# Performance work log

Hardware: AMD Instinct MI355X
Metric: run time of the kernel (lower is better)

Reference implementation:

```python
import jax, jax.numpy as jnp
import numpy as np

B, V, S, H = 16384, 16, 64, 512


def setup_inputs() -> dict:
    key = jax.random.key(0)
    kx, kw, kb, kws, kbs = jax.random.split(key, 5)
    x = jax.random.normal(kx, (B, V, S), dtype=jnp.float32)
    # per-variable linear layers: weight [V, S, H], bias [V, H]
    W = jax.random.normal(kw, (V, S, H), dtype=jnp.float32) * (1.0 / np.sqrt(S))
    b = jax.random.normal(kb, (V, H), dtype=jnp.float32) * 0.01
    # variable selection linear: hidden -> V
    W_sel = jax.random.normal(kws, (H, V), dtype=jnp.float32) * (1.0 / np.sqrt(H))
    b_sel = jax.random.normal(kbs, (V,), dtype=jnp.float32) * 0.01
    return {"x": x, "W": W, "b": b, "W_sel": W_sel, "b_sel": b_sel}


def reference(x, W, b, W_sel, b_sel):
    # per-variable linears: [B, V, H]
    transformed = jnp.einsum('bvs,vsh->bvh', x, W) + b  # grouped small GEMMs
    # torch stacks to [B, H, V]; mean over variable axis -> [B, H]
    flat = transformed.mean(axis=1)
    # softmax-gated selection weights [B, V] (dropout is identity in eval)
    weights = jax.nn.softmax(flat @ W_sel + b_sel, axis=-1)
    # weighted sum over variables -> [B, H]
    out = jnp.einsum('bvh,bv->bh', transformed, weights)
    return out
```

## Files before the change

kernel.cpp:

```cpp
#include <hip/hip_runtime.h>
#include <hip/hip_bf16.h>
#include <stdint.h>

#define B_ROWS 16384
#define VDIM   16
#define SDIM   64
#define HDIM   512
#define KDIM   1024
#define KP     1056
#define ASTR   1064
#define K2_LDS (64 * ASTR * 2)

using bf16x8 = __attribute__((ext_vector_type(8))) __bf16;
using u16x8  = __attribute__((ext_vector_type(8))) unsigned short;
using f32x4  = __attribute__((ext_vector_type(4))) float;

__device__ __forceinline__ unsigned short f2bf(float f) {
  unsigned int u = __builtin_bit_cast(unsigned int, f);
  u = (u + 0x7FFFu + ((u >> 16) & 1u)) >> 16;
  return (unsigned short)u;
}
__device__ __forceinline__ float bf2f(unsigned short s) {
  return __builtin_bit_cast(float, (unsigned int)s << 16);
}

__global__ __launch_bounds__(256) void k0_prep(
    const float* __restrict__ W, const float* __restrict__ bias,
    const float* __restrict__ Wsel, const float* __restrict__ bsel,
    unsigned short* __restrict__ Bt, unsigned short* __restrict__ WcombT,
    float* __restrict__ bcomb) {
  __shared__ float bm[HDIM];
  __shared__ float part[16][17];
  const int t = threadIdx.x;
  if (blockIdx.x < 2112) {
    int idx = blockIdx.x * 256 + t;
    int k = idx >> 9;
    int n = idx & 511;
    float val;
    if (k < KDIM)            val = W[(size_t)k * HDIM + n];
    else if (k < KDIM + 16)  val = bias[(size_t)(k - KDIM) * HDIM + n];
    else                     val = 0.f;
    Bt[(size_t)n * KP + k] = f2bf(val);
    return;
  }
  const int bid = blockIdx.x - 2112;
  if (bid < 256) {
    const int wave = t >> 6, lane = t & 63;
    const int k = bid * 4 + wave;
    const float* wr = W + (size_t)k * HDIM;
    float s[16];
    #pragma unroll
    for (int v = 0; v < 16; ++v) s[v] = 0.f;
    #pragma unroll
    for (int j = 0; j < 8; ++j) {
      const int h = lane + 64 * j;
      const float a = wr[h];
      const float4* wl = (const float4*)(Wsel + h * 16);
      const float4 q0 = wl[0], q1 = wl[1], q2 = wl[2], q3 = wl[3];
      s[0]  = fmaf(a, q0.x, s[0]);  s[1]  = fmaf(a, q0.y, s[1]);
      s[2]  = fmaf(a, q0.z, s[2]);  s[3]  = fmaf(a, q0.w, s[3]);
      s[4]  = fmaf(a, q1.x, s[4]);  s[5]  = fmaf(a, q1.y, s[5]);
      s[6]  = fmaf(a, q1.z, s[6]);  s[7]  = fmaf(a, q1.w, s[7]);
      s[8]  = fmaf(a, q2.x, s[8]);  s[9]  = fmaf(a, q2.y, s[9]);
      s[10] = fmaf(a, q2.z, s[10]); s[11] = fmaf(a, q2.w, s[11]);
      s[12] = fmaf(a, q3.x, s[12]); s[13] = fmaf(a, q3.y, s[13]);
      s[14] = fmaf(a, q3.z, s[14]); s[15] = fmaf(a, q3.w, s[15]);
    }
    #pragma unroll
    for (int off = 32; off > 0; off >>= 1) {
      #pragma unroll
      for (int v = 0; v < 16; ++v) s[v] += __shfl_xor(s[v], off, 64);
    }
    float mine = 0.f;
    #pragma unroll
    for (int v = 0; v < 16; ++v) mine = (lane == v) ? s[v] : mine;
    if (lane < 16) WcombT[lane * KDIM + k] = f2bf(mine * (1.f / 16.f));
  } else {
    for (int h = t; h < HDIM; h += 256) {
      float s = 0.f;
      #pragma unroll
      for (int v = 0; v < VDIM; ++v) s += bias[v * HDIM + h];
      bm[h] = s * (1.f / 16.f);
    }
    __syncthreads();
    int v = t & 15, sl = t >> 4;
    float s = 0.f;
    for (int h = sl * 32; h < sl * 32 + 32; ++h) s = fmaf(bm[h], Wsel[h * VDIM + v], s);
    part[sl][v] = s;
    __syncthreads();
    if (t < 16) {
      float s2 = bsel[t];
      #pragma unroll
      for (int i = 0; i < 16; ++i) s2 += part[i][t];
      bcomb[t] = s2;
    }
  }
}

__global__ __launch_bounds__(256) void k1a_logits(
    const float* __restrict__ x, const unsigned short* __restrict__ WcombT,
    float* __restrict__ part, unsigned short* __restrict__ xb) {
  const int gw = blockIdx.x * 4 + (threadIdx.x >> 6);
  const int lane = threadIdx.x & 63;
  const int rt = gw >> 2, seg = gw & 3;
  const int m = lane & 15, quad = lane >> 4;
  const size_t off0 = (size_t)(rt * 16 + m) * KDIM + seg * 256 + quad * 8;
  const float* xr = x + off0;
  unsigned short* xw = xb + off0;
  const unsigned short* br = WcombT + m * KDIM + seg * 256 + quad * 8;
  f32x4 acc = {0.f, 0.f, 0.f, 0.f};
  #pragma unroll
  for (int kt = 0; kt < 8; ++kt) {
    float4 a0 = *(const float4*)(xr);
    float4 a1 = *(const float4*)(xr + 4);
    xr += 32;
    u16x8 u;
    u[0] = f2bf(a0.x); u[1] = f2bf(a0.y); u[2] = f2bf(a0.z); u[3] = f2bf(a0.w);
    u[4] = f2bf(a1.x); u[5] = f2bf(a1.y); u[6] = f2bf(a1.z); u[7] = f2bf(a1.w);
    *(u16x8*)xw = u;
    xw += 32;
    bf16x8 af = __builtin_bit_cast(bf16x8, u);
    bf16x8 bfv = *(const bf16x8*)(br);
    br += 32;
    acc = __builtin_amdgcn_mfma_f32_16x16x32_bf16(af, bfv, acc, 0, 0, 0);
  }
  float* pr = part + (size_t)(rt * 16 + quad * 4) * 64 + seg * 16 + m;
  #pragma unroll
  for (int r = 0; r < 4; ++r) pr[(size_t)r * 64] = acc[r];
}

__global__ __launch_bounds__(256) void k1b0_softmax(
    const float* __restrict__ part, const float* __restrict__ bcomb,
    float* __restrict__ weights) {
  const int row = blockIdx.x * 256 + threadIdx.x;
  const float* p = part + (size_t)row * 64;
  float l[16];
  float mx = -1e30f;
  #pragma unroll
  for (int v = 0; v < 16; ++v) {
    l[v] = bcomb[v] + p[v] + p[16 + v] + p[32 + v] + p[48 + v];
    mx = fmaxf(mx, l[v]);
  }
  float s = 0.f;
  #pragma unroll
  for (int v = 0; v < 16; ++v) { l[v] = __expf(l[v] - mx); s += l[v]; }
  const float inv = 1.f / s;
  float4* wout = (float4*)(weights + (size_t)row * 16);
  #pragma unroll
  for (int q = 0; q < 4; ++q) {
    float4 f;
    f.x = l[4 * q + 0] * inv; f.y = l[4 * q + 1] * inv;
    f.z = l[4 * q + 2] * inv; f.w = l[4 * q + 3] * inv;
    wout[q] = f;
  }
}

__global__ __launch_bounds__(512, 2) void k2f_gemm(
    const unsigned short* __restrict__ xb, const float* __restrict__ wts,
    const unsigned short* __restrict__ Bt, float* __restrict__ C) {
  extern __shared__ unsigned short As[];

  const int t = threadIdx.x;
  const int rowb = blockIdx.x * 64;

  {
    const int srow = t >> 3;
    const int sc = (t & 7) * 8;
    const unsigned short* xr = xb + (size_t)(rowb + srow) * KDIM + sc;
    const float* wr = wts + (size_t)(rowb + srow) * 16;
    float wv[16];
    #pragma unroll
    for (int q = 0; q < 4; ++q) {
      float4 f = ((const float4*)wr)[q];
      wv[4 * q + 0] = f.x; wv[4 * q + 1] = f.y; wv[4 * q + 2] = f.z; wv[4 * q + 3] = f.w;
    }
    unsigned short* aw = As + srow * ASTR + sc;
    #pragma unroll 4
    for (int i = 0; i < 16; ++i) {
      const u16x8 a = *(const u16x8*)(xr + i * 64);
      const float w = wv[i];
      u16x8 o;
      #pragma unroll
      for (int j = 0; j < 8; ++j) o[j] = f2bf(w * bf2f(a[j]));
      *(u16x8*)(aw + i * 64) = o;
    }
    if ((t & 7) < 4) {
      const int j8 = (t & 7) * 8;
      unsigned short o[8];
      #pragma unroll
      for (int jj = 0; jj < 8; ++jj)
        o[jj] = (j8 + jj < 16) ? f2bf(wv[j8 + jj]) : (unsigned short)0;
      *(u16x8*)(As + srow * ASTR + KDIM + j8) = *(const u16x8*)o;
    }
  }

  const int wave = t >> 6, lane = t & 63;
  const int mlane = lane & 15, quad = lane >> 4;
  const int colb = wave * 64;

  const unsigned short* bp[4];
  #pragma unroll
  for (int j = 0; j < 4; ++j)
    bp[j] = Bt + (size_t)(colb + j * 16 + mlane) * KP + quad * 8;

  bf16x8 bv0[4], bv1[4];
  #pragma unroll
  for (int j = 0; j < 4; ++j) {
    bv0[j] = *(const bf16x8*)(bp[j]);
    bv1[j] = *(const bf16x8*)(bp[j] + 32);
    bp[j] += 64;
  }

  __syncthreads();

  const unsigned short* ap[4];
  #pragma unroll
  for (int i = 0; i < 4; ++i)
    ap[i] = As + (i * 16 + mlane) * ASTR + quad * 8;

  f32x4 acc[4][4];
  const f32x4 z = {0.f, 0.f, 0.f, 0.f};
  #pragma unroll
  for (int i = 0; i < 4; ++i)
    #pragma unroll
    for (int j = 0; j < 4; ++j) acc[i][j] = z;

  #pragma unroll 1
  for (int kt = 0; kt < 33; ++kt) {
    bf16x8 bnext[4];
    if (kt < 31) {
      #pragma unroll
      for (int j = 0; j < 4; ++j) { bnext[j] = *(const bf16x8*)bp[j]; bp[j] += 32; }
    }
    bf16x8 av[4];
    #pragma unroll
    for (int i = 0; i < 4; ++i) { av[i] = *(const bf16x8*)ap[i]; ap[i] += 32; }
    #pragma unroll
    for (int i = 0; i < 4; ++i)
      #pragma unroll
      for (int j = 0; j < 4; ++j)
        acc[i][j] = __builtin_amdgcn_mfma_f32_16x16x32_bf16(av[i], bv0[j], acc[i][j], 0, 0, 0);
    #pragma unroll
    for (int j = 0; j < 4; ++j) { bv0[j] = bv1[j]; bv1[j] = bnext[j]; }
  }

  #pragma unroll
  for (int i = 0; i < 4; ++i)
    #pragma unroll
    for (int j = 0; j < 4; ++j)
      #pragma unroll
      for (int r = 0; r < 4; ++r) {
        const size_t row = (size_t)rowb + i * 16 + quad * 4 + r;
        const int col = colb + j * 16 + mlane;
        C[row * HDIM + col] = acc[i][j][r];
      }
}

extern "C" void kernel_launch(void* const* d_in, const int* in_sizes, int n_in,
                              void* d_out, int out_size, void* d_ws, size_t ws_size,
                              hipStream_t stream) {
  const float* x    = (const float*)d_in[0];
  const float* W    = (const float*)d_in[1];
  const float* bias = (const float*)d_in[2];
  const float* Wsel = (const float*)d_in[3];
  const float* bsel = (const float*)d_in[4];
  float* out = (float*)d_out;

  char* ws = (char*)d_ws;
  unsigned short* Bt     = (unsigned short*)(ws);
  unsigned short* WcombT = (unsigned short*)(ws + 1081344);
  float*          bcomb  = (float*)(ws + 1114112);
  float*          part   = (float*)(ws + 1114368);
  float*          wts    = (float*)(ws + 5308672);
  unsigned short* xbb    = (unsigned short*)(ws + 6357248);

  static int lds_set = 0;
  if (!lds_set) {
    hipFuncSetAttribute((const void*)k2f_gemm,
                        hipFuncAttributeMaxDynamicSharedMemorySize, K2_LDS);
    lds_set = 1;
  }

  k0_prep<<<2369, 256, 0, stream>>>(W, bias, Wsel, bsel, Bt, WcombT, bcomb);
  k1a_logits<<<1024, 256, 0, stream>>>(x, WcombT, part, xbb);
  k1b0_softmax<<<64, 256, 0, stream>>>(part, bcomb, wts);
  k2f_gemm<<<256, 512, K2_LDS, stream>>>(xbb, wts, Bt, out);
}
```

Baseline: 162.9 us.

## Fuse logits, softmax and weighted GEMM into one kernel reading fp32 x

Measured after the change: 152.6 us. 6.3% less time.

```diff
diff --git a/kernel.cpp b/kernel.cpp
--- a/kernel.cpp
+++ b/kernel.cpp
@@ -9,7 +9,9 @@
 #define KDIM   1024
 #define KP     1056
 #define ASTR   1064
-#define K2_LDS (64 * ASTR * 2)
+#define PLOG_OFF 136192
+#define WLDS_OFF (136192 + 8704)
+#define K2_LDS   (136192 + 8704 + 4096)
 
 using bf16x8 = __attribute__((ext_vector_type(8))) __bf16;
 using u16x8  = __attribute__((ext_vector_type(8))) unsigned short;
@@ -97,88 +99,89 @@
   }
 }
 
-__global__ __launch_bounds__(256) void k1a_logits(
+__global__ __launch_bounds__(512, 2) void k2f_fused(
     const float* __restrict__ x, const unsigned short* __restrict__ WcombT,
-    float* __restrict__ part, unsigned short* __restrict__ xb) {
-  const int gw = blockIdx.x * 4 + (threadIdx.x >> 6);
-  const int lane = threadIdx.x & 63;
-  const int rt = gw >> 2, seg = gw & 3;
-  const int m = lane & 15, quad = lane >> 4;
-  const size_t off0 = (size_t)(rt * 16 + m) * KDIM + seg * 256 + quad * 8;
-  const float* xr = x + off0;
-  unsigned short* xw = xb + off0;
-  const unsigned short* br = WcombT + m * KDIM + seg * 256 + quad * 8;
-  f32x4 acc = {0.f, 0.f, 0.f, 0.f};
-  #pragma unroll
-  for (int kt = 0; kt < 8; ++kt) {
-    float4 a0 = *(const float4*)(xr);
-    float4 a1 = *(const float4*)(xr + 4);
-    xr += 32;
-    u16x8 u;
-    u[0] = f2bf(a0.x); u[1] = f2bf(a0.y); u[2] = f2bf(a0.z); u[3] = f2bf(a0.w);
-    u[4] = f2bf(a1.x); u[5] = f2bf(a1.y); u[6] = f2bf(a1.z); u[7] = f2bf(a1.w);
-    *(u16x8*)xw = u;
-    xw += 32;
-    bf16x8 af = __builtin_bit_cast(bf16x8, u);
-    bf16x8 bfv = *(const bf16x8*)(br);
-    br += 32;
-    acc = __builtin_amdgcn_mfma_f32_16x16x32_bf16(af, bfv, acc, 0, 0, 0);
-  }
-  float* pr = part + (size_t)(rt * 16 + quad * 4) * 64 + seg * 16 + m;
-  #pragma unroll
-  for (int r = 0; r < 4; ++r) pr[(size_t)r * 64] = acc[r];
-}
-
-__global__ __launch_bounds__(256) void k1b0_softmax(
-    const float* __restrict__ part, const float* __restrict__ bcomb,
-    float* __restrict__ weights) {
-  const int row = blockIdx.x * 256 + threadIdx.x;
-  const float* p = part + (size_t)row * 64;
-  float l[16];
-  float mx = -1e30f;
-  #pragma unroll
-  for (int v = 0; v < 16; ++v) {
-    l[v] = bcomb[v] + p[v] + p[16 + v] + p[32 + v] + p[48 + v];
-    mx = fmaxf(mx, l[v]);
-  }
-  float s = 0.f;
-  #pragma unroll
-  for (int v = 0; v < 16; ++v) { l[v] = __expf(l[v] - mx); s += l[v]; }
-  const float inv = 1.f / s;
-  float4* wout = (float4*)(weights + (size_t)row * 16);
-  #pragma unroll
-  for (int q = 0; q < 4; ++q) {
-    float4 f;
-    f.x = l[4 * q + 0] * inv; f.y = l[4 * q + 1] * inv;
-    f.z = l[4 * q + 2] * inv; f.w = l[4 * q + 3] * inv;
-    wout[q] = f;
-  }
-}
-
-__global__ __launch_bounds__(512, 2) void k2f_gemm(
-    const unsigned short* __restrict__ xb, const float* __restrict__ wts,
-    const unsigned short* __restrict__ Bt, float* __restrict__ C) {
+    const float* __restrict__ bcomb, const unsigned short* __restrict__ Bt,
+    float* __restrict__ C) {
   extern __shared__ unsigned short As[];
+  float* plog = (float*)((char*)As + PLOG_OFF);
+  float* wlds = (float*)((char*)As + WLDS_OFF);
 
   const int t = threadIdx.x;
   const int rowb = blockIdx.x * 64;
-
+  const int wave = t >> 6, lane = t & 63;
+  const int mlane = lane & 15, quad = lane >> 4;
+
+  const int srow = t >> 3;
+  const int sc = (t & 7) * 8;
+  u16x8 xreg[16];
   {
-    const int srow = t >> 3;
-    const int sc = (t & 7) * 8;
-    const unsigned short* xr = xb + (size_t)(rowb + srow) * KDIM + sc;
-    const float* wr = wts + (size_t)(rowb + srow) * 16;
-    float wv[16];
-    #pragma unroll
-    for (int q = 0; q < 4; ++q) {
-      float4 f = ((const float4*)wr)[q];
-      wv[4 * q + 0] = f.x; wv[4 * q + 1] = f.y; wv[4 * q + 2] = f.z; wv[4 * q + 3] = f.w;
-    }
+    const float* xr = x + (size_t)(rowb + srow) * KDIM + sc;
     unsigned short* aw = As + srow * ASTR + sc;
     #pragma unroll 4
     for (int i = 0; i < 16; ++i) {
-      const u16x8 a = *(const u16x8*)(xr + i * 64);
+      const float4 a0 = *(const float4*)(xr + i * 64);
+      const float4 a1 = *(const float4*)(xr + i * 64 + 4);
+      u16x8 u;
+      u[0] = f2bf(a0.x); u[1] = f2bf(a0.y); u[2] = f2bf(a0.z); u[3] = f2bf(a0.w);
+      u[4] = f2bf(a1.x); u[5] = f2bf(a1.y); u[6] = f2bf(a1.z); u[7] = f2bf(a1.w);
+      xreg[i] = u;
+      *(u16x8*)(aw + i * 64) = u;
+    }
+  }
+  __syncthreads();
+
+  {
+    const int kh = wave >> 2, rg = wave & 3;
+    const unsigned short* al = As + (rg * 16 + mlane) * ASTR + kh * 512 + quad * 8;
+    const unsigned short* bl = WcombT + mlane * KDIM + kh * 512 + quad * 8;
+    f32x4 acc = {0.f, 0.f, 0.f, 0.f};
+    #pragma unroll
+    for (int kt = 0; kt < 16; ++kt) {
+      bf16x8 a = *(const bf16x8*)al; al += 32;
+      bf16x8 b = *(const bf16x8*)bl; bl += 32;
+      acc = __builtin_amdgcn_mfma_f32_16x16x32_bf16(a, b, acc, 0, 0, 0);
+    }
+    float* pl = plog + ((size_t)((kh * 4 + rg) * 16 + quad * 4) * 17 + mlane);
+    #pragma unroll
+    for (int r = 0; r < 4; ++r) pl[r * 17] = acc[r];
+  }
+  __syncthreads();
+
+  if (t < 64) {
+    const int rg = t >> 4, r = t & 15;
+    const float* p0 = plog + ((size_t)(rg * 16 + r) * 17);
+    const float* p1 = plog + ((size_t)((4 + rg) * 16 + r) * 17);
+    float l[16];
+    float mx = -1e30f;
+    #pragma unroll
+    for (int v = 0; v < 16; ++v) {
+      l[v] = p0[v] + p1[v] + bcomb[v];
+      mx = fmaxf(mx, l[v]);
+    }
+    float s = 0.f;
+    #pragma unroll
+    for (int v = 0; v < 16; ++v) { l[v] = __expf(l[v] - mx); s += l[v]; }
+    const float inv = 1.f / s;
+    float* wo = wlds + t * 16;
+    #pragma unroll
+    for (int v = 0; v < 16; ++v) wo[v] = l[v] * inv;
+  }
+  __syncthreads();
+
+  {
+    float wv[16];
+    const float4* wq = (const float4*)(wlds + srow * 16);
+    #pragma unroll
+    for (int q = 0; q < 4; ++q) {
+      const float4 f = wq[q];
+      wv[4 * q + 0] = f.x; wv[4 * q + 1] = f.y; wv[4 * q + 2] = f.z; wv[4 * q + 3] = f.w;
+    }
+    unsigned short* aw = As + srow * ASTR + sc;
+    #pragma unroll 4
+    for (int i = 0; i < 16; ++i) {
       const float w = wv[i];
+      const u16x8 a = xreg[i];
       u16x8 o;
       #pragma unroll
       for (int j = 0; j < 8; ++j) o[j] = f2bf(w * bf2f(a[j]));
@@ -194,10 +197,7 @@
     }
   }
 
-  const int wave = t >> 6, lane = t & 63;
-  const int mlane = lane & 15, quad = lane >> 4;
   const int colb = wave * 64;
-
   const unsigned short* bp[4];
   #pragma unroll
   for (int j = 0; j < 4; ++j)
@@ -270,19 +270,14 @@
   unsigned short* Bt     = (unsigned short*)(ws);
   unsigned short* WcombT = (unsigned short*)(ws + 1081344);
   float*          bcomb  = (float*)(ws + 1114112);
-  float*          part   = (float*)(ws + 1114368);
-  float*          wts    = (float*)(ws + 5308672);
-  unsigned short* xbb    = (unsigned short*)(ws + 6357248);
 
   static int lds_set = 0;
   if (!lds_set) {
-    hipFuncSetAttribute((const void*)k2f_gemm,
+    hipFuncSetAttribute((const void*)k2f_fused,
                         hipFuncAttributeMaxDynamicSharedMemorySize, K2_LDS);
     lds_set = 1;
   }
 
   k0_prep<<<2369, 256, 0, stream>>>(W, bias, Wsel, bsel, Bt, WcombT, bcomb);
-  k1a_logits<<<1024, 256, 0, stream>>>(x, WcombT, part, xbb);
-  k1b0_softmax<<<64, 256, 0, stream>>>(part, bcomb, wts);
-  k2f_gemm<<<256, 512, K2_LDS, stream>>>(xbb, wts, Bt, out);
-}
+  k2f_fused<<<256, 512, K2_LDS, stream>>>(x, WcombT, bcomb, Bt, out);
+}
```
